# Kernel optimization log

Hardware: AMD Instinct MI355X
Metric: run time of the kernel (lower is better)

The kernel has to match this reference:

```python
import jax, jax.numpy as jnp
import numpy as np
import math

B, N, HID = 2, 2048, 768
H, D = 12, HID // 12


def _rel_shift(x):
    # x: [i, j, b, h] -- Transformer-XL relative shift via zero-pad + reshape
    i, j = x.shape[0], x.shape[1]
    zero_pad = jnp.zeros((i, 1) + x.shape[2:], x.dtype)
    x_padded = jnp.concatenate([zero_pad, x], axis=1)  # [i, j+1, b, h]
    x_padded = x_padded.reshape((j + 1, i) + x.shape[2:])
    return x_padded[1:].reshape(x.shape)


def setup_inputs() -> dict:
    key = jax.random.key(0)
    ks = jax.random.split(key, 10)
    inp = {
        "hidden_states": jax.random.normal(ks[0], (B, N, HID), dtype=jnp.float32),
        "r_emb": jax.random.normal(ks[1], (N, H, D), dtype=jnp.float32) * 0.02,
        "r_w_bias": jax.random.normal(ks[2], (H, D), dtype=jnp.float32) * 0.02,
        "r_bias": jax.random.normal(ks[3], (N, H), dtype=jnp.float32) * 0.02,
        "Wq": jax.random.normal(ks[4], (HID, HID), dtype=jnp.float32) * 0.02,
        "bq": jnp.zeros((HID,), dtype=jnp.float32),
        "Wk": jax.random.normal(ks[5], (HID, HID), dtype=jnp.float32) * 0.02,
        "bk": jnp.zeros((HID,), dtype=jnp.float32),
        "Wv": jax.random.normal(ks[6], (HID, HID), dtype=jnp.float32) * 0.02,
        "bv": jnp.zeros((HID,), dtype=jnp.float32),
    }
    return inp


def reference(hidden_states, r_emb, r_w_bias, r_bias, Wq, bq, Wk, bk, Wv, bv):
    b, n, hid = hidden_states.shape
    h, d = r_w_bias.shape
    # projections (torch Linear: x @ W.T + b)
    q = (hidden_states @ Wq.T + bq).reshape(b, n, h, d).transpose(1, 0, 2, 3)  # [n,b,h,d]
    k = (hidden_states @ Wk.T + bk).reshape(b, n, h, d).transpose(1, 0, 2, 3)  # [n,b,h,d]
    v = (hidden_states @ Wv.T + bv).reshape(b, n, h, d).transpose(0, 2, 1, 3)  # [b,h,n,d]
    # r_emb/r_bias sliced to last n positions (already length n here)
    re = r_emb[-n:]
    rb = r_bias[-n:]
    rw_head_q = q + r_w_bias  # broadcast [h,d] over [n,b,h,d]
    AC = jnp.einsum('ibnd,jbnd->ijbn', rw_head_q, k)          # [n,n,b,h]
    BD = jnp.einsum('ibnd,jnd->ijbn', q, re) + rb[None, :, None, :]
    BD = _rel_shift(BD)
    scores = (AC + BD).transpose(2, 3, 0, 1) / math.sqrt(d)    # [b,h,n,n]
    probs = jax.nn.softmax(scores, axis=-1)
    ctx = jnp.einsum('bhij,bhjd->bhid', probs, v)              # [b,h,n,d]
    out = ctx.transpose(0, 2, 1, 3).reshape(b, n, h * d)       # [b,n,hid]
    return out
```

## Files before the change

kernel.cpp:

```cpp
#include <hip/hip_runtime.h>
#include <math.h>

constexpr int B   = 2;
constexpr int N   = 2048;
constexpr int HID = 768;
constexpr int H   = 12;
constexpr int D   = 64;
constexpr int M   = B * N;
constexpr int QKV_ELEMS = B * H * N * D;

typedef __attribute__((ext_vector_type(8))) short s8v;
typedef __attribute__((ext_vector_type(8))) unsigned short u8v;
typedef __attribute__((ext_vector_type(4))) float f4v;
typedef unsigned short ushort_t;

__device__ __forceinline__ float bf2f(short u) {
    union { unsigned int i; float f; } v;
    v.i = ((unsigned int)(unsigned short)u) << 16;
    return v.f;
}
__device__ __forceinline__ unsigned short f2bf(float f) {
    union { float f; unsigned int i; } v; v.f = f;
    unsigned int r = v.i + 0x7fff + ((v.i >> 16) & 1);
    return (unsigned short)(r >> 16);
}
__device__ __forceinline__ unsigned short f2bf_fast(float f) {
    union { float f; unsigned int i; } v; v.f = f;
    return (unsigned short)((v.i + 0x8000u) >> 16);
}
__device__ __forceinline__ float exp2raw(float x) {
    float r;
    asm("v_exp_f32 %0, %1" : "=v"(r) : "v"(x));
    return r;
}
__device__ __forceinline__ f4v mfma16(s8v a, s8v b, f4v c) {
    return __builtin_amdgcn_mfma_f32_16x16x32_bf16(a, b, c, 0, 0, 0);
}
__device__ __forceinline__ void gl2lds16(const void* g, void* l) {
    __builtin_amdgcn_global_load_lds(
        (const __attribute__((address_space(1))) void*)g,
        (__attribute__((address_space(3))) void*)l, 16, 0, 0);
}
__device__ __forceinline__ u8v cvt8(const float* src) {
    float4 a = *(const float4*)src;
    float4 b = *(const float4*)(src + 4);
    u8v o;
    o[0] = f2bf(a.x); o[1] = f2bf(a.y); o[2] = f2bf(a.z); o[3] = f2bf(a.w);
    o[4] = f2bf(b.x); o[5] = f2bf(b.y); o[6] = f2bf(b.z); o[7] = f2bf(b.w);
    return o;
}
__device__ __forceinline__ int clampsrc(int tv) {
    int src = (tv < 0) ? tv + N : tv;
    return (src < 0) ? 0 : ((src > N - 1) ? N - 1 : src);
}
__device__ __forceinline__ int swz64(int row, int c8) {
    return (row << 6) + ((c8 ^ (row & 7)) << 3);
}

#define SCL 0.18033688011112042f

constexpr int CVT_C0 = M * HID / 8;
constexpr int CVT_C1 = CVT_C0 + 3 * HID * HID / 8;
constexpr int CVT_C2 = CVT_C1 + H * N * D / 8;
constexpr int CVT_C3 = CVT_C2 + H * N;

__global__ __launch_bounds__(256) void convert_kernel(
    const float* __restrict__ hs,
    const float* __restrict__ Wq, const float* __restrict__ Wk,
    const float* __restrict__ Wv,
    const float* __restrict__ r_emb, const float* __restrict__ r_bias,
    ushort_t* __restrict__ hsb, ushort_t* __restrict__ Wb,
    ushort_t* __restrict__ reb, float* __restrict__ rbt)
{
    const int idx = blockIdx.x * 256 + threadIdx.x;
    if (idx < CVT_C0) {
        *(u8v*)&hsb[(size_t)idx * 8] = cvt8(&hs[(size_t)idx * 8]);
    } else if (idx < CVT_C1) {
        const int j  = idx - CVT_C0;
        const int z  = j / (HID * HID / 8);
        const int jj = j - z * (HID * HID / 8);
        const float* W = (z == 0) ? Wq : ((z == 1) ? Wk : Wv);
        *(u8v*)&Wb[(size_t)z * HID * HID + (size_t)jj * 8] =
            cvt8(&W[(size_t)jj * 8]);
    } else if (idx < CVT_C2) {
        const int k  = idx - CVT_C1;
        const int d0 = (k & 7) * 8;
        const int s  = (k >> 3) & (N - 1);
        const int h  = k >> 14;
        *(u8v*)&reb[(size_t)k * 8] = cvt8(&r_emb[((size_t)s * H + h) * D + d0]);
    } else if (idx < CVT_C3) {
        const int j = idx - CVT_C2;
        const int h = j >> 11;
        const int s = j & (N - 1);
        rbt[j] = r_bias[(size_t)s * H + h];
    }
}

__global__ __launch_bounds__(256) void qkv_mfma_kernel(
    const ushort_t* __restrict__ hsb, const ushort_t* __restrict__ Wb,
    const float* __restrict__ bq, const float* __restrict__ bk,
    const float* __restrict__ bv,
    ushort_t* __restrict__ Qo, ushort_t* __restrict__ Ko,
    ushort_t* __restrict__ Vt)
{
    const int z  = blockIdx.z;
    const int m0 = blockIdx.x * 128;
    const int o0 = blockIdx.y * 128;
    const ushort_t* Wz = Wb + (size_t)z * HID * HID;
    const float* bias = (z == 0) ? bq : ((z == 1) ? bk : bv);

    __shared__ ushort_t Ah[128 * 64];
    __shared__ ushort_t Wh[128 * 64];

    const int t    = threadIdx.x;
    const int lane = t & 63;
    const int w    = t >> 6;
    const int quad = lane >> 4;
    const int col  = lane & 15;
    const int x0   = (w >> 1) * 64;
    const int y0   = (w & 1) * 64;

    const ushort_t* Xs = (z == 2) ? Ah : Wh;
    const ushort_t* Ys = (z == 2) ? Wh : Ah;

    f4v acc[16];
    #pragma unroll
    for (int i = 0; i < 16; i++) acc[i] = (f4v){0.f, 0.f, 0.f, 0.f};

    const int srow = w * 32 + (lane >> 3);
    const int scol = lane & 7;

    for (int k0 = 0; k0 < HID; k0 += 64) {
        __syncthreads();
        #pragma unroll
        for (int e = 0; e < 4; e++) {
            const int row = srow + e * 8;
            const int c8  = scol ^ (row & 7);
            gl2lds16(&hsb[(size_t)(m0 + row) * HID + k0 + c8 * 8],
                     (void*)&Ah[(w * 32 + e * 8) * 64]);
            gl2lds16(&Wz[(size_t)(o0 + row) * HID + k0 + c8 * 8],
                     (void*)&Wh[(w * 32 + e * 8) * 64]);
        }
        __syncthreads();

        #pragma unroll
        for (int ks = 0; ks < 2; ks++) {
            s8v xf[4], yf[4];
            #pragma unroll
            for (int tt = 0; tt < 4; tt++) {
                const int xr  = x0 + tt * 16 + col;
                const int xc8 = (ks * 4 + quad) ^ (xr & 7);
                xf[tt] = *(const s8v*)&Xs[xr * 64 + xc8 * 8];
                const int yr  = y0 + tt * 16 + col;
                const int yc8 = (ks * 4 + quad) ^ (yr & 7);
                yf[tt] = *(const s8v*)&Ys[yr * 64 + yc8 * 8];
            }
            #pragma unroll
            for (int xt = 0; xt < 4; xt++)
                #pragma unroll
                for (int yt = 0; yt < 4; yt++)
                    acc[xt * 4 + yt] = mfma16(xf[xt], yf[yt], acc[xt * 4 + yt]);
        }
    }

    if (z < 2) {
        ushort_t* dst = (z == 0) ? Qo : Ko;
        #pragma unroll
        for (int xt = 0; xt < 4; xt++) {
            const int ob = o0 + x0 + xt * 16 + quad * 4;
            const int h  = ob >> 6;
            const int d0 = ob & 63;
            const float4 bv4 = *(const float4*)&bias[ob];
            #pragma unroll
            for (int yt = 0; yt < 4; yt++) {
                const int m  = m0 + y0 + yt * 16 + col;
                const int bb = m >> 11;
                const int ii = m & (N - 1);
                f4v a = acc[xt * 4 + yt];
                ushort4 pk;
                pk.x = f2bf(a[0] + bv4.x);
                pk.y = f2bf(a[1] + bv4.y);
                pk.z = f2bf(a[2] + bv4.z);
                pk.w = f2bf(a[3] + bv4.w);
                *(ushort4*)&dst[(((size_t)bb * H + h) * N + ii) * D + d0] = pk;
            }
        }
    } else {
        #pragma unroll
        for (int yt = 0; yt < 4; yt++) {
            const int o = o0 + y0 + yt * 16 + col;
            const int h = o >> 6;
            const int d = o & 63;
            const float bs = bias[o];
            #pragma unroll
            for (int xt = 0; xt < 4; xt++) {
                const int m  = m0 + x0 + xt * 16 + quad * 4;
                const int bb = m >> 11;
                const int ib = m & (N - 1);
                f4v a = acc[xt * 4 + yt];
                ushort4 pk;
                pk.x = f2bf(a[0] + bs);
                pk.y = f2bf(a[1] + bs);
                pk.z = f2bf(a[2] + bs);
                pk.w = f2bf(a[3] + bs);
                *(ushort4*)&Vt[(((size_t)bb * H + h) * D + d) * N + ib] = pk;
            }
        }
    }
}

__global__ __launch_bounds__(256, 3) void attn_mfma_kernel(
    const ushort_t* __restrict__ Qb, const ushort_t* __restrict__ Kb,
    const ushort_t* __restrict__ Vt, const ushort_t* __restrict__ reb,
    const float* __restrict__ rbt, const float* __restrict__ rwb_g,
    float* __restrict__ out)
{
    const int i0 = blockIdx.x * 64;
    const int h  = blockIdx.y;
    const int b  = blockIdx.z;
    const int bh = b * H + h;

    const ushort_t* Qbh = Qb + (size_t)bh * N * D;
    const ushort_t* Kbh = Kb + (size_t)bh * N * D;
    const ushort_t* Vbh = Vt + (size_t)bh * D * N;
    const ushort_t* reh = reb + (size_t)h * N * D;
    const float*    rbh = rbt + (size_t)h * N;

    __shared__ __align__(16) char smem[51712];
    ushort_t* Ks  = (ushort_t*)(smem + 0);
    ushort_t* Vs  = (ushort_t*)(smem + 8192);
    ushort_t* Res = (ushort_t*)(smem + 16384);
    ushort_t (*SbT)[72] = (ushort_t(*)[72])(smem + 32768);
    float*    Rb        = (float*)(smem + 41984);
    ushort_t (*QL)[72]  = (ushort_t(*)[72])(smem + 42496);
    ushort_t (*PsAll)[72] = (ushort_t(*)[72])(smem + 42496);

    const int t    = threadIdx.x;
    const int lane = t & 63;
    const int w    = t >> 6;
    const int quad = lane >> 4;
    const int col  = lane & 15;
    ushort_t (*Ps)[72] = PsAll + w * 16;

    #pragma unroll
    for (int e = 0; e < 2; e++) {
        const int idx = t + e * 256;
        const int r   = idx >> 3;
        const int d8  = (idx & 7) * 8;
        *(s8v*)&QL[r][d8] = *(const s8v*)&Qbh[(size_t)(i0 + r) * D + d8];
    }
    const int sub = t & 3;
    float q64f[16];
    {
        s8v q64a = {0,0,0,0,0,0,0,0}, q64b = {0,0,0,0,0,0,0,0};
        if (i0 + 64 < N) {
            q64a = *(const s8v*)&Qbh[(size_t)(i0 + 64) * D + sub * 16];
            q64b = *(const s8v*)&Qbh[(size_t)(i0 + 64) * D + sub * 16 + 8];
        }
        #pragma unroll
        for (int j = 0; j < 8; j++) {
            q64f[j]     = bf2f(q64a[j]) * SCL;
            q64f[j + 8] = bf2f(q64b[j]) * SCL;
        }
    }
    __syncthreads();

    s8v qr[2], qw[2];
    #pragma unroll
    for (int ks = 0; ks < 2; ks++) {
        s8v qraw = *(s8v*)&QL[16 * w + col][ks * 32 + quad * 8];
        float4 r0 = *(const float4*)&rwb_g[h * D + ks * 32 + quad * 8];
        float4 r1 = *(const float4*)&rwb_g[h * D + ks * 32 + quad * 8 + 4];
        const float rv[8] = {r0.x, r0.y, r0.z, r0.w, r1.x, r1.y, r1.z, r1.w};
        s8v qq, qs;
        #pragma unroll
        for (int j = 0; j < 8; j++) {
            const float qf = bf2f(qraw[j]);
            qs[j] = (short)f2bf(qf * SCL);
            qq[j] = (short)f2bf((qf + rv[j]) * SCL);
        }
        qr[ks] = qs;
        qw[ks] = qq;
    }

    {
        #pragma unroll
        for (int e = 0; e < 2; e++) {
            const int idx = t + e * 256;
            const int r   = idx >> 3;
            const int c8  = idx & 7;
            *(s8v*)&Ks[swz64(r, c8)] = *(const s8v*)&Kbh[(size_t)r * D + c8 * 8];
            *(s8v*)&Vs[swz64(r, c8)] = *(const s8v*)&Vbh[(size_t)r * N + c8 * 8];
        }
        #pragma unroll
        for (int e = 0; e < 4; e++) {
            const int idx = t + e * 256;
            const int u   = idx >> 3;
            const int c8  = idx & 7;
            const int src = clampsrc(u - i0 - 65);
            *(s8v*)&Res[swz64(u, c8)] = *(const s8v*)&reh[(size_t)src * D + c8 * 8];
        }
        if (t < 128) Rb[t] = rbh[clampsrc(t - i0 - 65)] * SCL;
    }

    f4v Oacc[4];
    #pragma unroll
    for (int dt = 0; dt < 4; dt++) Oacc[dt] = (f4v){0.f, 0.f, 0.f, 0.f};
    float lacc[4] = {0.f, 0.f, 0.f, 0.f};

    const int u0w  = 48 - 16 * w;
    const int u64  = 16 * w + (lane >> 2);
    int off = 0;

    const int r0pf = t >> 3;
    const int d8pf = (t & 7) * 8;
    const ushort_t* pK = Kbh + (size_t)(64 + r0pf) * D + d8pf;
    const ushort_t* pV = Vbh + (size_t)r0pf * N + 64 + d8pf;
    int reBase = 64 - i0 - 1;

    for (int s = 0; s < 32; ++s) {
        const int j0 = s * 64;
        __syncthreads();

        s8v pk[2], pv[2], pr[2];
        float prb = 0.f;
        if (s < 31) {
            #pragma unroll
            for (int e = 0; e < 2; e++) {
                pk[e] = *(const s8v*)(pK + (size_t)e * 32 * D);
                pv[e] = *(const s8v*)(pV + (size_t)e * 32 * N);
                const int src = clampsrc(reBase + r0pf + e * 32);
                pr[e] = *(const s8v*)&reh[(size_t)src * D + d8pf];
            }
            if (t < 64) prb = rbh[clampsrc(reBase + t)] * SCL;
        }

        __builtin_amdgcn_s_setprio(1);
        f4v acc[4];
        #pragma unroll
        for (int tile = 0; tile < 4; tile++) {
            acc[tile] = (f4v){0.f, 0.f, 0.f, 0.f};
            #pragma unroll
            for (int ks = 0; ks < 2; ks++) {
                s8v kb = *(s8v*)&Ks[swz64(tile * 16 + col, ks * 4 + quad)];
                acc[tile] = mfma16(qw[ks], kb, acc[tile]);
            }
        }
        #pragma unroll
        for (int tt = 0; tt < 5; tt++) {
            const int u = u0w + tt * 16 + col;
            const float rbv = Rb[(u + off) & 127];
            f4v sb = (f4v){rbv, rbv, rbv, rbv};
            #pragma unroll
            for (int ks = 0; ks < 2; ks++) {
                s8v rb8 = *(s8v*)&Res[swz64((u + off) & 127, ks * 4 + quad)];
                sb = mfma16(qr[ks], rb8, sb);
            }
            #pragma unroll
            for (int reg = 0; reg < 4; reg++) {
                const int rho = 16 * w + quad * 4 + reg;
                const int row = tt * 16 + col + quad * 4 + reg - 16;
                if ((unsigned)row < 64u)
                    SbT[row][rho] = f2bf_fast(sb[reg]);
            }
        }
        __builtin_amdgcn_s_setprio(0);
        {
            float part = 0.f;
            const int rp = (u64 + off) & 127;
            s8v r0 = *(s8v*)&Res[swz64(rp, sub * 2)];
            s8v r1 = *(s8v*)&Res[swz64(rp, sub * 2 + 1)];
            #pragma unroll
            for (int j = 0; j < 8; j++) {
                part += q64f[j]     * bf2f(r0[j]);
                part += q64f[j + 8] * bf2f(r1[j]);
            }
            part += __shfl_xor(part, 1, 64);
            part += __shfl_xor(part, 2, 64);
            if (sub == 0)
                SbT[u64][64] = f2bf_fast(part + Rb[rp]);
        }
        __syncthreads();

        float p[4][4];
        const int rbase = 16 * w + quad * 4;
        #pragma unroll
        for (int tile = 0; tile < 4; tile++) {
            const int cr   = tile * 16 + col;
            ushort4 q4a = *(ushort4*)&SbT[cr][rbase];
            ushort_t b4 = SbT[cr][rbase + 4];
            float vf[5];
            vf[0] = bf2f((short)q4a.x); vf[1] = bf2f((short)q4a.y);
            vf[2] = bf2f((short)q4a.z); vf[3] = bf2f((short)q4a.w);
            vf[4] = bf2f((short)b4);
            const int c = (j0 + tile * 16 + col) - (i0 + rbase) - 2;
            #pragma unroll
            for (int reg = 0; reg < 4; reg++) {
                float bd = (reg <= c) ? vf[reg + 1] : vf[reg];
                bd = (c == reg - 1) ? 0.f : bd;
                const float e = exp2raw(acc[tile][reg] + bd);
                p[tile][reg] = e;
                lacc[reg] += e;
            }
        }
        #pragma unroll
        for (int tile = 0; tile < 4; tile++)
            #pragma unroll
            for (int reg = 0; reg < 4; reg++)
                Ps[quad * 4 + reg][tile * 16 + col] = f2bf_fast(p[tile][reg]);
        __asm__ volatile("s_waitcnt lgkmcnt(0)" ::: "memory");
        __builtin_amdgcn_s_setprio(1);
        #pragma unroll
        for (int dt = 0; dt < 4; dt++) {
            #pragma unroll
            for (int ks = 0; ks < 2; ks++) {
                s8v pf = *(s8v*)&Ps[col][ks * 32 + quad * 8];
                s8v vf = *(s8v*)&Vs[swz64(dt * 16 + col, ks * 4 + quad)];
                Oacc[dt] = mfma16(pf, vf, Oacc[dt]);
            }
        }
        __builtin_amdgcn_s_setprio(0);
        __syncthreads();

        if (s < 31) {
            #pragma unroll
            for (int e = 0; e < 2; e++) {
                const int idx = t + e * 256;
                const int r   = idx >> 3;
                const int c8  = idx & 7;
                *(s8v*)&Ks[swz64(r, c8)] = pk[e];
                *(s8v*)&Vs[swz64(r, c8)] = pv[e];
                *(s8v*)&Res[swz64((r + off) & 127, c8)] = pr[e];
            }
            if (t < 64) Rb[(t + off) & 127] = prb;
            off = (off + 64) & 127;
            pK += (size_t)64 * D;
            pV += 64;
            reBase += 64;
        }
    }

    #pragma unroll
    for (int reg = 0; reg < 4; reg++) {
        #pragma unroll
        for (int msk = 1; msk < 16; msk <<= 1)
            lacc[reg] += __shfl_xor(lacc[reg], msk, 64);
    }
    #pragma unroll
    for (int reg = 0; reg < 4; reg++) {
        const float inv = 1.f / lacc[reg];
        const int row = i0 + 16 * w + quad * 4 + reg;
        const size_t base = ((size_t)b * N + row) * HID + h * D;
        #pragma unroll
        for (int dt = 0; dt < 4; dt++)
            out[base + dt * 16 + col] = Oacc[dt][reg] * inv;
    }
}

extern "C" void kernel_launch(void* const* d_in, const int* in_sizes, int n_in,
                              void* d_out, int out_size, void* d_ws, size_t ws_size,
                              hipStream_t stream)
{
    (void)in_sizes; (void)n_in; (void)out_size; (void)ws_size;
    const float* hs   = (const float*)d_in[0];
    const float* remb = (const float*)d_in[1];
    const float* rwb  = (const float*)d_in[2];
    const float* rb   = (const float*)d_in[3];
    const float* Wq   = (const float*)d_in[4];
    const float* bq   = (const float*)d_in[5];
    const float* Wk   = (const float*)d_in[6];
    const float* bk   = (const float*)d_in[7];
    const float* Wv   = (const float*)d_in[8];
    const float* bv   = (const float*)d_in[9];
    float* out = (float*)d_out;

    ushort_t* Qb  = (ushort_t*)d_ws;
    ushort_t* Kb  = Qb + QKV_ELEMS;
    ushort_t* Vt  = Kb + QKV_ELEMS;
    ushort_t* reb = Vt + QKV_ELEMS;
    float*    rbt = (float*)(reb + H * N * D);
    ushort_t* hsb = (ushort_t*)(rbt + H * N);
    ushort_t* Wb  = hsb + (size_t)M * HID;

    convert_kernel<<<CVT_C3 / 256, 256, 0, stream>>>(
        hs, Wq, Wk, Wv, remb, rb, hsb, Wb, reb, rbt);
    qkv_mfma_kernel<<<dim3(M / 128, HID / 128, 3), 256, 0, stream>>>(
        hsb, Wb, bq, bk, bv, Qb, Kb, Vt);
    attn_mfma_kernel<<<dim3(N / 64, H, B), 256, 0, stream>>>(
        Qb, Kb, Vt, reb, rbt, rwb, out);
}
```

Measured before the change: 226.9 us.

## Load K/V fragments directly to registers, async-copy rel-emb to LDS, remap block order

Drops the K and V shared-memory tiles. Each lane now loads its MFMA operand fragments for K and V straight from global memory into registers, with K prefetched one iteration ahead. The relative-embedding tile is written into LDS with direct global-to-LDS copies (gl2lds16) using a pre-swizzled source address, and one barrier per iteration is removed. Block IDs are remapped so that consecutive blocks are spread across batch-head groups, which is meant to improve L2 and XCD locality. The change cuts LDS use and register staging, in exchange for redundant uncoalesced global loads of K and V across waves and V loads that are not prefetched.

```diff
diff --git a/kernel.cpp b/kernel.cpp
--- a/kernel.cpp
+++ b/kernel.cpp
@@ -215,10 +215,13 @@
     const float* __restrict__ rbt, const float* __restrict__ rwb_g,
     float* __restrict__ out)
 {
-    const int i0 = blockIdx.x * 64;
-    const int h  = blockIdx.y;
-    const int b  = blockIdx.z;
-    const int bh = b * H + h;
+    const int fid  = blockIdx.x + 32 * (blockIdx.y + 12 * blockIdx.z);
+    const int work = (fid & 7) * 96 + (fid >> 3);
+    const int i0   = (work & 31) * 64;
+    const int hb   = work >> 5;
+    const int b    = (hb >= 12) ? 1 : 0;
+    const int h    = hb - 12 * b;
+    const int bh   = b * H + h;
 
     const ushort_t* Qbh = Qb + (size_t)bh * N * D;
     const ushort_t* Kbh = Kb + (size_t)bh * N * D;
@@ -226,14 +229,12 @@
     const ushort_t* reh = reb + (size_t)h * N * D;
     const float*    rbh = rbt + (size_t)h * N;
 
-    __shared__ __align__(16) char smem[51712];
-    ushort_t* Ks  = (ushort_t*)(smem + 0);
-    ushort_t* Vs  = (ushort_t*)(smem + 8192);
-    ushort_t* Res = (ushort_t*)(smem + 16384);
-    ushort_t (*SbT)[72] = (ushort_t(*)[72])(smem + 32768);
-    float*    Rb        = (float*)(smem + 41984);
-    ushort_t (*QL)[72]  = (ushort_t(*)[72])(smem + 42496);
-    ushort_t (*PsAll)[72] = (ushort_t(*)[72])(smem + 42496);
+    __shared__ __align__(16) char smem[35328];
+    ushort_t* Res = (ushort_t*)(smem);
+    ushort_t (*SbT)[72] = (ushort_t(*)[72])(smem + 16384);
+    float*    Rb        = (float*)(smem + 25600);
+    ushort_t (*QL)[72]  = (ushort_t(*)[72])(smem + 26112);
+    ushort_t (*PsAll)[72] = (ushort_t(*)[72])(smem + 26112);
 
     const int t    = threadIdx.x;
     const int lane = t & 63;
@@ -250,18 +251,10 @@
         *(s8v*)&QL[r][d8] = *(const s8v*)&Qbh[(size_t)(i0 + r) * D + d8];
     }
     const int sub = t & 3;
-    float q64f[16];
-    {
-        s8v q64a = {0,0,0,0,0,0,0,0}, q64b = {0,0,0,0,0,0,0,0};
-        if (i0 + 64 < N) {
-            q64a = *(const s8v*)&Qbh[(size_t)(i0 + 64) * D + sub * 16];
-            q64b = *(const s8v*)&Qbh[(size_t)(i0 + 64) * D + sub * 16 + 8];
-        }
-        #pragma unroll
-        for (int j = 0; j < 8; j++) {
-            q64f[j]     = bf2f(q64a[j]) * SCL;
-            q64f[j + 8] = bf2f(q64b[j]) * SCL;
-        }
+    s8v q64a = {0,0,0,0,0,0,0,0}, q64b = {0,0,0,0,0,0,0,0};
+    if (i0 + 64 < N) {
+        q64a = *(const s8v*)&Qbh[(size_t)(i0 + 64) * D + sub * 16];
+        q64b = *(const s8v*)&Qbh[(size_t)(i0 + 64) * D + sub * 16 + 8];
     }
     __syncthreads();
 
@@ -283,25 +276,31 @@
         qw[ks] = qq;
     }
 
+    const ushort_t* bK = Kbh + (size_t)col * D + quad * 8;
+    const ushort_t* bV[4];
+    #pragma unroll
+    for (int dt = 0; dt < 4; dt++)
+        bV[dt] = Vbh + (size_t)(dt * 16 + col) * N + quad * 8;
+
     {
         #pragma unroll
-        for (int e = 0; e < 2; e++) {
-            const int idx = t + e * 256;
-            const int r   = idx >> 3;
-            const int c8  = idx & 7;
-            *(s8v*)&Ks[swz64(r, c8)] = *(const s8v*)&Kbh[(size_t)r * D + c8 * 8];
-            *(s8v*)&Vs[swz64(r, c8)] = *(const s8v*)&Vbh[(size_t)r * N + c8 * 8];
-        }
-        #pragma unroll
         for (int e = 0; e < 4; e++) {
-            const int idx = t + e * 256;
-            const int u   = idx >> 3;
-            const int c8  = idx & 7;
-            const int src = clampsrc(u - i0 - 65);
-            *(s8v*)&Res[swz64(u, c8)] = *(const s8v*)&reh[(size_t)src * D + c8 * 8];
+            const int rb_ = w * 8 + e * 32;
+            const int r   = rb_ + (lane >> 3);
+            const int c8  = lane & 7;
+            const int src = clampsrc(r - i0 - 65);
+            gl2lds16(&reh[(size_t)src * D + ((c8 ^ (r & 7)) * 8)],
+                     (void*)&Res[rb_ * 64]);
         }
         if (t < 128) Rb[t] = rbh[clampsrc(t - i0 - 65)] * SCL;
     }
+    s8v kr[8];
+    #pragma unroll
+    for (int tile = 0; tile < 4; tile++)
+        #pragma unroll
+        for (int ks = 0; ks < 2; ks++)
+            kr[tile * 2 + ks] = *(const s8v*)(bK + tile * 16 * D + ks * 32);
+    __syncthreads();
 
     f4v Oacc[4];
     #pragma unroll
@@ -311,29 +310,13 @@
     const int u0w  = 48 - 16 * w;
     const int u64  = 16 * w + (lane >> 2);
     int off = 0;
-
-    const int r0pf = t >> 3;
-    const int d8pf = (t & 7) * 8;
-    const ushort_t* pK = Kbh + (size_t)(64 + r0pf) * D + d8pf;
-    const ushort_t* pV = Vbh + (size_t)r0pf * N + 64 + d8pf;
     int reBase = 64 - i0 - 1;
 
     for (int s = 0; s < 32; ++s) {
         const int j0 = s * 64;
-        __syncthreads();
-
-        s8v pk[2], pv[2], pr[2];
+
         float prb = 0.f;
-        if (s < 31) {
-            #pragma unroll
-            for (int e = 0; e < 2; e++) {
-                pk[e] = *(const s8v*)(pK + (size_t)e * 32 * D);
-                pv[e] = *(const s8v*)(pV + (size_t)e * 32 * N);
-                const int src = clampsrc(reBase + r0pf + e * 32);
-                pr[e] = *(const s8v*)&reh[(size_t)src * D + d8pf];
-            }
-            if (t < 64) prb = rbh[clampsrc(reBase + t)] * SCL;
-        }
+        if (s < 31 && t < 64) prb = rbh[clampsrc(reBase + t)] * SCL;
 
         __builtin_amdgcn_s_setprio(1);
         f4v acc[4];
@@ -341,10 +324,8 @@
         for (int tile = 0; tile < 4; tile++) {
             acc[tile] = (f4v){0.f, 0.f, 0.f, 0.f};
             #pragma unroll
-            for (int ks = 0; ks < 2; ks++) {
-                s8v kb = *(s8v*)&Ks[swz64(tile * 16 + col, ks * 4 + quad)];
-                acc[tile] = mfma16(qw[ks], kb, acc[tile]);
-            }
+            for (int ks = 0; ks < 2; ks++)
+                acc[tile] = mfma16(qw[ks], kr[tile * 2 + ks], acc[tile]);
         }
         #pragma unroll
         for (int tt = 0; tt < 5; tt++) {
@@ -372,15 +353,35 @@
             s8v r1 = *(s8v*)&Res[swz64(rp, sub * 2 + 1)];
             #pragma unroll
             for (int j = 0; j < 8; j++) {
-                part += q64f[j]     * bf2f(r0[j]);
-                part += q64f[j + 8] * bf2f(r1[j]);
+                part += bf2f(q64a[j]) * bf2f(r0[j]);
+                part += bf2f(q64b[j]) * bf2f(r1[j]);
             }
             part += __shfl_xor(part, 1, 64);
             part += __shfl_xor(part, 2, 64);
             if (sub == 0)
-                SbT[u64][64] = f2bf_fast(part + Rb[rp]);
+                SbT[u64][64] = f2bf_fast(part * SCL + Rb[rp]);
         }
         __syncthreads();
+
+        s8v vr[8];
+        #pragma unroll
+        for (int dt = 0; dt < 4; dt++)
+            #pragma unroll
+            for (int ks = 0; ks < 2; ks++)
+                vr[dt * 2 + ks] = *(const s8v*)(bV[dt] + ks * 32);
+
+        if (s < 31) {
+            #pragma unroll
+            for (int e = 0; e < 2; e++) {
+                const int rb_ = w * 8 + e * 32;
+                const int r   = rb_ + (lane >> 3);
+                const int c8  = lane & 7;
+                const int src = clampsrc(reBase + r);
+                gl2lds16(&reh[(size_t)src * D + ((c8 ^ (r & 7)) * 8)],
+                         (void*)&Res[((rb_ + off) & 127) * 64]);
+            }
+            if (t < 64) Rb[(t + off) & 127] = prb;
+        }
 
         float p[4][4];
         const int rbase = 16 * w + quad * 4;
@@ -408,6 +409,15 @@
             #pragma unroll
             for (int reg = 0; reg < 4; reg++)
                 Ps[quad * 4 + reg][tile * 16 + col] = f2bf_fast(p[tile][reg]);
+        if (s < 31) {
+            bK += (size_t)64 * D;
+            #pragma unroll
+            for (int tile = 0; tile < 4; tile++)
+                #pragma unroll
+                for (int ks = 0; ks < 2; ks++)
+                    kr[tile * 2 + ks] =
+                        *(const s8v*)(bK + tile * 16 * D + ks * 32);
+        }
         __asm__ volatile("s_waitcnt lgkmcnt(0)" ::: "memory");
         __builtin_amdgcn_s_setprio(1);
         #pragma unroll
@@ -415,27 +425,16 @@
             #pragma unroll
             for (int ks = 0; ks < 2; ks++) {
                 s8v pf = *(s8v*)&Ps[col][ks * 32 + quad * 8];
-                s8v vf = *(s8v*)&Vs[swz64(dt * 16 + col, ks * 4 + quad)];
-                Oacc[dt] = mfma16(pf, vf, Oacc[dt]);
+                Oacc[dt] = mfma16(pf, vr[dt * 2 + ks], Oacc[dt]);
             }
         }
         __builtin_amdgcn_s_setprio(0);
         __syncthreads();
 
         if (s < 31) {
-            #pragma unroll
-            for (int e = 0; e < 2; e++) {
-                const int idx = t + e * 256;
-                const int r   = idx >> 3;
-                const int c8  = idx & 7;
-                *(s8v*)&Ks[swz64(r, c8)] = pk[e];
-                *(s8v*)&Vs[swz64(r, c8)] = pv[e];
-                *(s8v*)&Res[swz64((r + off) & 127, c8)] = pr[e];
-            }
-            if (t < 64) Rb[(t + off) & 127] = prb;
             off = (off + 64) & 127;
-            pK += (size_t)64 * D;
-            pV += 64;
+            #pragma unroll
+            for (int dt = 0; dt < 4; dt++) bV[dt] += 64;
             reBase += 64;
         }
     }
```

Result: slower. 338.1 us (+49.0%).
